# Kernel optimization log

Measured on AMD Instinct MI355X. Metric: run time of the kernel, lower is better.

Reference implementation:

```python
import jax, jax.numpy as jnp
import numpy as np

# ---- fixed configuration (see shape_source) ----
B, ND, NPR = 64, 32, 32          # batch, drug-subgraph nodes, protein-subgraph nodes
LD, LP = 100, 1000               # drug_MAX_LENGH, protein_MAX_LENGH
DIM, CONV = 64, 40               # char_dim, conv
DK, PK = (4, 6, 8), (4, 8, 12)   # drug_kernel, protein_kernel
VD, VP = 71, 26                  # SMILES / FASTA vocab sizes
ED, EP, EDP = 128, 128, 64       # DDI / PPI / DPI edges per subgraph
GNN_LAYERS = 2
SLOPE = 0.01                     # LeakyReLU default slope


def setup_inputs():
    key = jax.random.key(0)
    ks = iter(jax.random.split(key, 64))
    def nrm(shape, s=0.02):
        return jax.random.normal(next(ks), shape, jnp.float32) * s
    inp = {}
    inp['drug_tokens'] = jax.random.randint(next(ks), (B, LD), 0, VD, jnp.int32)
    inp['protein_tokens'] = jax.random.randint(next(ks), (B, LP), 0, VP, jnp.int32)
    inp['drug_node_tokens'] = jax.random.randint(next(ks), (B, ND, LD), 0, VD, jnp.int32)
    inp['protein_node_tokens'] = jax.random.randint(next(ks), (B, NPR, LP), 0, VP, jnp.int32)
    inp['ddi_edges'] = jax.random.randint(next(ks), (B, 2, ED), 0, ND, jnp.int32)
    inp['ppi_edges'] = jax.random.randint(next(ks), (B, 2, EP), 0, NPR, jnp.int32)
    inp['dpi_edges'] = jax.random.randint(next(ks), (B, 2, EDP), 0, min(ND, NPR), jnp.int32)
    # sequence embeddings (padding_idx=0 -> zero row)
    inp['drug_embed'] = nrm((VD, DIM)).at[0].set(0.)
    inp['protein_embed'] = nrm((VP, DIM)).at[0].set(0.)
    # drug CNN stack
    inp['dW1'], inp['db1'] = nrm((CONV, DIM, DK[0])), jnp.zeros((CONV,), jnp.float32)
    inp['dW2'], inp['db2'] = nrm((2*CONV, CONV, DK[1])), jnp.zeros((2*CONV,), jnp.float32)
    inp['dW3'], inp['db3'] = nrm((4*CONV, 2*CONV, DK[2])), jnp.zeros((4*CONV,), jnp.float32)
    # protein CNN stack
    inp['pW1'], inp['pb1'] = nrm((CONV, DIM, PK[0])), jnp.zeros((CONV,), jnp.float32)
    inp['pW2'], inp['pb2'] = nrm((2*CONV, CONV, PK[1])), jnp.zeros((2*CONV,), jnp.float32)
    inp['pW3'], inp['pb3'] = nrm((4*CONV, 2*CONV, PK[2])), jnp.zeros((4*CONV,), jnp.float32)
    # graph node-feature embedding tables (creat_drug_node / creat_protein_node)
    inp['drug_node_table'] = nrm((VD, LD)).at[0].set(0.)
    inp['protein_node_table'] = nrm((VP, LP)).at[0].set(0.)
    # SAGEConv params: Wl (neighbor path, has bias), Wr (root path, no bias)
    inp['ddi_Wl'], inp['ddi_bl'], inp['ddi_Wr'] = nrm((LD, LD)), jnp.zeros((LD,), jnp.float32), nrm((LD, LD))
    inp['ppi_Wl'], inp['ppi_bl'], inp['ppi_Wr'] = nrm((LP, LP)), jnp.zeros((LP,), jnp.float32), nrm((LP, LP))
    inp['dpi_Wl'], inp['dpi_bl'], inp['dpi_Wr'] = nrm((LP, LD)), jnp.zeros((LP,), jnp.float32), nrm((LP, LP))
    inp['pdi_Wl'], inp['pdi_bl'], inp['pdi_Wr'] = nrm((LD, LP)), jnp.zeros((LD,), jnp.float32), nrm((LD, LD))
    # fusion MLP
    inp['fc1_W'], inp['fc1_b'] = nrm((1024, 1420)), jnp.zeros((1024,), jnp.float32)
    inp['fc2_W'], inp['fc2_b'] = nrm((1024, 1024)), jnp.zeros((1024,), jnp.float32)
    inp['fc3_W'], inp['fc3_b'] = nrm((512, 1024)), jnp.zeros((512,), jnp.float32)
    inp['out_W'], inp['out_b'] = nrm((2, 512)), jnp.zeros((2,), jnp.float32)
    return inp


def _conv_relu(x, w, b):
    # x: [B, Cin, L], w: [Cout, Cin, K] -> valid Conv1d + ReLU
    y = jax.lax.conv_general_dilated(x, w, (1,), 'VALID',
                                     dimension_numbers=('NCH', 'OIH', 'NCH'))
    return jax.nn.relu(y + b[None, :, None])


def _node_feat(tokens, table, vocab):
    # mean over sequence of embedded tokens == (token-count histogram / L) @ table
    counts = jax.nn.one_hot(tokens, vocab, dtype=table.dtype).sum(axis=2)  # [B, N, V]
    return jnp.einsum('bnv,vd->bnd', counts, table) / tokens.shape[-1]


def _sage(xs, xd, edges, Wl, bl, Wr):
    # PyG SAGEConv, aggr='mean': lin_l(mean_j x_src[j]) + lin_r(x_dst)
    src, dst = edges[0], edges[1]
    n = xd.shape[0]
    s = jax.ops.segment_sum(xs[src], dst, num_segments=n)
    c = jax.ops.segment_sum(jnp.ones((src.shape[0],), xs.dtype), dst, num_segments=n)
    agg = s / jnp.maximum(c, 1.0)[:, None]
    return agg @ Wl.T + bl + xd @ Wr.T


def _forward(drug_tokens, protein_tokens, drug_node_tokens, protein_node_tokens,
             ddi_edges, ppi_edges, dpi_edges,
             drug_embed, protein_embed,
             dW1, db1, dW2, db2, dW3, db3,
             pW1, pb1, pW2, pb2, pW3, pb3,
             drug_node_table, protein_node_table,
             ddi_Wl, ddi_bl, ddi_Wr, ppi_Wl, ppi_bl, ppi_Wr,
             dpi_Wl, dpi_bl, dpi_Wr, pdi_Wl, pdi_bl, pdi_Wr,
             fc1_W, fc1_b, fc2_W, fc2_b, fc3_W, fc3_b, out_W, out_b):
    # --- CNN branches (maxpool kernel spans whole remaining length == global max) ---
    x = drug_embed[drug_tokens].transpose(0, 2, 1)            # [B, DIM, LD]
    for w, b in ((dW1, db1), (dW2, db2), (dW3, db3)):
        x = _conv_relu(x, w, b)
    drug_feat = x.max(axis=2)                                 # [B, 4*CONV]
    y = protein_embed[protein_tokens].transpose(0, 2, 1)      # [B, DIM, LP]
    for w, b in ((pW1, pb1), (pW2, pb2), (pW3, pb3)):
        y = _conv_relu(y, w, b)
    prot_feat = y.max(axis=2)                                 # [B, 4*CONV]
    # --- graph node features: mean over sequence of node-token embeddings ---
    dx = _node_feat(drug_node_tokens, drug_node_table, VD)    # [B, ND, LD]
    px = _node_feat(protein_node_tokens, protein_node_table, VP)  # [B, NPR, LP]
    # --- hetero SAGE message passing, aggr='mean' across relations ---
    def _hetero(dxi, pxi, ddi, ppi, dpi):
        pdi = dpi[::-1]
        d = 0.5 * (_sage(dxi, dxi, ddi, ddi_Wl, ddi_bl, ddi_Wr)
                   + _sage(pxi, dxi, pdi, pdi_Wl, pdi_bl, pdi_Wr))
        p = 0.5 * (_sage(pxi, pxi, ppi, ppi_Wl, ppi_bl, ppi_Wr)
                   + _sage(dxi, pxi, dpi, dpi_Wl, dpi_bl, dpi_Wr))
        return d, p
    hetero_b = jax.vmap(_hetero)
    for _ in range(GNN_LAYERS):
        dx, px = hetero_b(dx, px, ddi_edges, ppi_edges, dpi_edges)
    # node 0 of each subgraph is the query drug / protein
    graph_feat = jnp.concatenate([dx[:, 0], px[:, 0]], axis=-1)   # [B, LD+LP]
    # --- fusion MLP (dropout = identity at eval) ---
    pair = jnp.concatenate([drug_feat, prot_feat, graph_feat], axis=-1)  # [B, 1420]
    h = jax.nn.leaky_relu(pair @ fc1_W.T + fc1_b, SLOPE)
    h = jax.nn.leaky_relu(h @ fc2_W.T + fc2_b, SLOPE)
    h = jax.nn.leaky_relu(h @ fc3_W.T + fc3_b, SLOPE)
    return h @ out_W.T + out_b                                 # [B, 2]


def reference(drug_tokens, protein_tokens, drug_node_tokens, protein_node_tokens,
              ddi_edges, ppi_edges, dpi_edges,
              drug_embed, protein_embed,
              dW1, db1, dW2, db2, dW3, db3,
              pW1, pb1, pW2, pb2, pW3, pb3,
              drug_node_table, protein_node_table,
              ddi_Wl, ddi_bl, ddi_Wr, ppi_Wl, ppi_bl, ppi_Wr,
              dpi_Wl, dpi_bl, dpi_Wr, pdi_Wl, pdi_bl, pdi_Wr,
              fc1_W, fc1_b, fc2_W, fc2_b, fc3_W, fc3_b, out_W, out_b):
    return _forward(drug_tokens, protein_tokens, drug_node_tokens, protein_node_tokens,
                    ddi_edges, ppi_edges, dpi_edges,
                    drug_embed, protein_embed,
                    dW1, db1, dW2, db2, dW3, db3,
                    pW1, pb1, pW2, pb2, pW3, pb3,
                    drug_node_table, protein_node_table,
                    ddi_Wl, ddi_bl, ddi_Wr, ppi_Wl, ppi_bl, ppi_Wr,
                    dpi_Wl, dpi_bl, dpi_Wr, pdi_Wl, pdi_bl, pdi_Wr,
                    fc1_W, fc1_b, fc2_W, fc2_b, fc3_W, fc3_b, out_W, out_b)
```

## Files before the change

### kernel.cpp

```cpp
#include <hip/hip_runtime.h>
#include <hip/hip_bf16.h>


typedef __attribute__((ext_vector_type(8))) short short8;
typedef __attribute__((ext_vector_type(4))) float f32x4;
union FragU { uint32_t u[4]; uint4 q; short8 s; };

static __device__ inline unsigned short f2bf(float v) {
    __hip_bfloat16 h = __float2bfloat16(v);
    return *(unsigned short*)&h;
}

static constexpr size_t O_PAIR = 0;
static constexpr size_t O_CF1  = 363520;
static constexpr size_t O_CF2  = 625664;
static constexpr size_t O_CF3  = 887808;
static constexpr size_t O_BD   = 1018880;
static constexpr size_t O_BP   = 1019392;
static constexpr size_t O_WDS  = 1023488;
static constexpr size_t O_WPS  = 1342976;
static constexpr size_t O_WTP1 = 5864960;
static constexpr size_t O_WTP2 = 5930496;
static constexpr size_t O_WTP3 = 6012416;
static constexpr size_t O_WTD1 = 6503936;
static constexpr size_t O_WTD2 = 6569472;
static constexpr size_t O_WTD3 = 6651392;
static constexpr size_t AR     = 6897152;
static constexpr size_t A_AD  = AR + 0;
static constexpr size_t A_AP  = AR + 479232;
static constexpr size_t A_A2D = AR + 1327104;
static constexpr size_t A_A2P = AR + 1486848;
static constexpr size_t A_UD  = AR + 1769472;
static constexpr size_t A_UP  = AR + 1855488;
static constexpr size_t A_RHO = AR + 2641920;
static constexpr size_t A_Y2P = AR + 0;
static constexpr size_t A_Y1P = AR + 10158080;
static constexpr size_t A_Y1D = AR + 15278080;
static constexpr size_t A_Y2D = AR + 15810560;
static constexpr size_t NEED_BYTES = AR + 16793600;

__global__ void zero32_k(uint32_t* __restrict__ p, int n) {
    int i = blockIdx.x * 256 + threadIdx.x;
    if (i < n) p[i] = 0u;
}

static constexpr long Q0 = 100;
static constexpr long Q1 = Q0 + 1000;
static constexpr long Q2 = Q1 + 14336;
static constexpr long Q3 = Q2 + 14336;
static constexpr long Q4 = Q3 + 131072;
static constexpr long Q5 = Q4 + 1048576;
static constexpr long Q6 = Q5 + 1048576;
static constexpr long Q7 = Q6 + 163840;
static constexpr long Q8 = Q7 + 32768;
static constexpr long Q9 = Q8 + 40960;
static constexpr long Q10 = Q9 + 245760;
static constexpr long Q11 = Q10 + 32768;
static constexpr long Q12 = Q11 + 40960;
static constexpr long Q13 = Q12 + 122880;
static constexpr long Q14 = Q13 + 70400;
static constexpr long Q15 = Q14 + 20480;
static constexpr long Q16 = Q15 + 163840;
// ... 43 lines not shown
    if (idx < Q8)  { wtconv_block(WtP1, pW1, 40, 64, 4, 8, idx - Q7); return; }
    if (idx < Q9)  { wtconv_block(WtP2, pW2, 80, 40, 8, 8, idx - Q8); return; }
    if (idx < Q10) { wtconv_block(WtP3, pW3, 160, 80, 12, 16, idx - Q9); return; }
    if (idx < Q11) { wtconv_block(WtD1, dW1, 40, 64, 4, 8, idx - Q10); return; }
    if (idx < Q12) { wtconv_block(WtD2, dW2, 80, 40, 6, 8, idx - Q11); return; }
    if (idx < Q13) { wtconv_block(WtD3, dW3, 160, 80, 8, 8, idx - Q12); return; }
    if (idx < Q14) {
        long l = idx - Q13;
        int b = (int)(l / 1100), j = (int)(l % 1100);
        if (j < 100) pair[(size_t)b * 1420 + 320 + j] = 0.5f * (ddi_bl[j] + pdi_bl[j]);
        else { int j2 = j - 100; pair[(size_t)b * 1420 + 420 + j2] = 0.5f * (ppi_bl[j2] + dpi_bl[j2]); }
        return;
    }
    if (idx < Q15) {
        long l = idx - Q14;
        int b = (int)(l / 320), j = (int)(l % 320);
        pair[(size_t)b * 1420 + j] = 0.f;
        return;
    }
    if (idx < Q16) { cfz[idx - Q15] = 0.f; return; }
    if (idx < Q17) { gnnz[idx - Q16] = 0u; return; }
}

__global__ __launch_bounds__(256) void gnn_front_k(const int* __restrict__ ddi,
                                                   const int* __restrict__ ppi,
                                                   const int* __restrict__ dpi,
                                                   const int* __restrict__ dtoks,
                                                   const int* __restrict__ ptoks,
                                                   const float* __restrict__ dtable,
                                                   const float* __restrict__ ptable,
                                                   float* __restrict__ RHO,
                                                   unsigned short* __restrict__ Ad,
                                                   unsigned short* __restrict__ Ap) {
    const int role = blockIdx.x, b = blockIdx.y, tid = threadIdx.x;
    __shared__ float M[4][32][32];
    __shared__ int cnt4[4][32];
    __shared__ float inv4[4][32];
    __shared__ float W7[7][32];
    __shared__ int cnt[32][72];
    __shared__ float WC[7][72];
    for (int i = tid; i < 4 * 32 * 32; i += 256) ((float*)M)[i] = 0.f;
    if (tid < 128) ((int*)cnt4)[tid] = 0;
    __syncthreads();
    const int* ed = ddi + (size_t)b * 256;
    const int* ep = ppi + (size_t)b * 256;
    const int* ex = dpi + (size_t)b * 128;
    if (tid < 128) {
        atomicAdd(&cnt4[0][ed[128 + tid]], 1);
        atomicAdd(&cnt4[1][ep[128 + tid]], 1);
    } else if (tid < 192) {
        int e = tid - 128;
        atomicAdd(&cnt4[2][ex[e]], 1);
        atomicAdd(&cnt4[3][ex[64 + e]], 1);
    }
    __syncthreads();
    if (tid < 128) {
        int which = tid >> 5, j = tid & 31;
        inv4[which][j] = 1.f / (float)max(cnt4[which][j], 1);
    }
    __syncthreads();
    if (tid < 128) {
        int s = ed[tid], d = ed[128 + tid];
        atomicAdd(&M[0][d][s], inv4[0][d]);
        int s2 = ep[tid], d2 = ep[128 + tid];
        atomicAdd(&M[1][d2][s2], inv4[1][d2]);
    } else if (tid < 192) {
        int e = tid - 128;
        int dr = ex[e], pr = ex[64 + e];
        atomicAdd(&M[2][dr][pr], inv4[2][dr]);
        atomicAdd(&M[3][pr][dr], inv4[3][pr]);
    }
    __syncthreads();
    if (tid < 32) {
        int j = tid;
        if (role == 0) {
            float r1 = 0.f, r4 = 0.f, r5 = 0.f, r7 = 0.f;
            for (int k = 0; k < 32; ++k) {
                r1 += M[0][0][k] * M[0][k][j];
                r4 += M[2][0][k] * M[3][k][j];
                r5 += M[1][0][k] * M[3][k][j];
                r7 += M[3][0][k] * M[0][k][j];
            }
            W7[0][j] = r1; W7[1][j] = M[0][0][j]; W7[2][j] = (j == 0) ? 1.f : 0.f;
            W7[3][j] = r4; W7[4][j] = r5; W7[5][j] = M[3][0][j]; W7[6][j] = r7;
        } else {
            float s1 = 0.f, s3 = 0.f, s4 = 0.f, s7 = 0.f;
            for (int k = 0; k < 32; ++k) {
                s1 += M[0][0][k] * M[2][k][j];
                s3 += M[2][0][k] * M[1][k][j];
                s4 += M[1][0][k] * M[1][k][j];
                s7 += M[3][0][k] * M[2][k][j];
            }
            W7[0][j] = s1; W7[1][j] = M[2][0][j]; W7[2][j] = s3;
            W7[3][j] = s4; W7[4][j] = M[1][0][j];
            W7[5][j] = (j == 0) ? 1.f : 0.f; W7[6][j] = s7;
        }
    }
    if (role == 0 && tid == 0) {
        float a = 0.f, bq = 0.f, cq = 0.f, dq = 0.f;
        for (int k = 0; k < 32; ++k) {
            a += M[0][0][k]; bq += M[2][0][k]; cq += M[1][0][k]; dq += M[3][0][k];
        }
        RHO[b * 4 + 0] = a; RHO[b * 4 + 1] = bq; RHO[b * 4 + 2] = cq; RHO[b * 4 + 3] = dq;
    }
    const int V = role ? 26 : 71;
    const int L = role ? 1000 : 100;
    for (int i = tid; i < 32 * 72; i += 256) ((int*)cnt)[i] = 0;
    __syncthreads();
    const int* tk = (role ? ptoks : dtoks) + (size_t)b * 32 * L;
    for (int i = tid; i < 32 * L; i += 256) atomicAdd(&cnt[i / L][tk[i]], 1);
    __syncthreads();
    float invL = 1.f / (float)L;
    for (int o = tid; o < 7 * V; o += 256) {
        int i = o / V, v = o % V;
        float a = 0.f;
        for (int k = 0; k < 32; ++k) a += W7[i][k] * (float)cnt[k][v];
        WC[i][v] = a * invL;
    }
    __syncthreads();
    size_t g0d = (size_t)b * 1248, g1d_ = (size_t)(64 + b) * 1248, g2d = (size_t)(128 + b) * 1248;
    size_t g0p = (size_t)b * 2208, g1p = (size_t)(64 + b) * 2208, g2p = (size_t)(128 + b) * 2208;
    if (role == 0) {
        int d = tid;
        if (d >= 100) return;
        float acc[7] = {};
        for (int v = 0; v < 71; ++v) {
            float tv = dtable[(size_t)v * 100 + d];
            #pragma unroll
            for (int i = 0; i < 7; ++i) acc[i] += WC[i][v] * tv;
        }
        unsigned short h;
        h = f2bf(acc[0]); Ad[g0d + d] = h;
        h = f2bf(acc[1]); Ad[g0d + 112 + d] = h; Ad[g1d_ + d] = h;
        h = f2bf(acc[2]); Ad[g1d_ + 112 + d] = h;
        h = f2bf(acc[3]); Ap[g0p + 2048 + d] = h;
        h = f2bf(acc[4]); Ap[g1p + 2048 + d] = h;
        h = f2bf(acc[5]); Ap[g2p + 2048 + d] = h; Ad[g2d + 112 + d] = h;
        h = f2bf(acc[6]); Ad[g2d + d] = h;
    } else {
        for (int d = tid; d < 1000; d += 256) {
            float acc[7] = {};
            for (int v = 0; v < 26; ++v) {
                float tv = ptable[(size_t)v * 1000 + d];
                #pragma unroll
                for (int i = 0; i < 7; ++i) acc[i] += WC[i][v] * tv;
            }
            unsigned short h;
            h = f2bf(acc[0]); Ad[g0d + 224 + d] = h;
            h = f2bf(acc[1]); Ad[g1d_ + 224 + d] = h; Ap[g0p + 1024 + d] = h;
            h = f2bf(acc[2]); Ap[g0p + d] = h;
            h = f2bf(acc[3]); Ap[g1p + d] = h;
            h = f2bf(acc[4]); Ap[g1p + 1024 + d] = h; Ap[g2p + d] = h;
            h = f2bf(acc[5]); Ap[g2p + 1024 + d] = h;
            h = f2bf(acc[6]); Ad[g2d + 224 + d] = h;
        }
    }
}

__device__ __forceinline__ void sk_body(const unsigned short* __restrict__ A, int lda,
                                        const unsigned short* __restrict__ Bm, int ldb,
                                        int K, int KS, float scale,
                                        float* __restrict__ out,
                                        int rs, int coloff, int Nw,
                                        int bx, int by, int gz) {
    const int tid = threadIdx.x;
    const int lane = tid & 63, w = tid >> 6, c = lane & 15, q = lane >> 4;
    const int n = bx * 64 + w * 16 + c;
    const unsigned short* Ab = A + (size_t)gz * 64 * lda;
// ... 3 lines not shown
    f32x4 acc[4];
    #pragma unroll
    for (int i = 0; i < 4; ++i) acc[i] = (f32x4){0.f, 0.f, 0.f, 0.f};
    for (int k = k0; k < k1; k += 32) {
        FragU bf;
        bf.q = *(const uint4*)&Bm[(size_t)n * ldb + k + q * 8];
        #pragma unroll
        for (int i = 0; i < 4; ++i) {
            FragU af;
            af.q = *(const uint4*)&Ab[(size_t)(i * 16 + c) * lda + k + q * 8];
            acc[i] = __builtin_amdgcn_mfma_f32_16x16x32_bf16(af.s, bf.s, acc[i], 0, 0, 0);
        }
    }
    if (n >= Nw) return;
    #pragma unroll
    for (int i = 0; i < 4; ++i)
        #pragma unroll
        for (int r = 0; r < 4; ++r) {
            int m = gz * 64 + i * 16 + q * 4 + r;
            atomicAdd(&out[(size_t)m * rs + coloff + n], scale * acc[i][r]);
        }
}

__global__ __launch_bounds__(256) void sk_stage1(const unsigned short* __restrict__ Ad,
                                                 const unsigned short* __restrict__ WdS,
                                                 float* __restrict__ Ud,
                                                 const unsigned short* __restrict__ Ap,
                                                 const unsigned short* __restrict__ WpS,
                                                 float* __restrict__ Up) {
    int z = blockIdx.z;
    if (z < 3) {
        sk_body(Ap, 2208, WpS, 2208, 2208, 8, 0.5f, Up, 1024, 0, 1000,
                blockIdx.x, blockIdx.y, z);
    } else {
        if (blockIdx.x >= 2) return;
        sk_body(Ad, 1248, WdS, 1248, 1248, 8, 0.5f, Ud, 112, 0, 100,
                blockIdx.x, blockIdx.y, z - 3);
    }
}

__global__ __launch_bounds__(256) void sk_stage2(const unsigned short* __restrict__ A2d,
                                                 const unsigned short* __restrict__ WdS,
                                                 const unsigned short* __restrict__ A2p,
                                                 const unsigned short* __restrict__ WpS,
                                                 float* __restrict__ pair) {
    int z = blockIdx.z;
    if (z == 0) {
        sk_body(A2p, 2208, WpS, 2208, 2208, 8, 0.5f, pair, 1420, 420, 1000,
                blockIdx.x, blockIdx.y, 0);
    } else {
        if (blockIdx.x >= 2) return;
        sk_body(A2d, 1248, WdS, 1248, 1248, 8, 0.5f, pair, 1420, 320, 100,
                blockIdx.x, blockIdx.y, 0);
    }
}

__global__ void ep_k(const float* __restrict__ Ud, const float* __restrict__ Up,
                     const float* __restrict__ RHO,
                     const float* __restrict__ bd, const float* __restrict__ bp,
                     unsigned short* __restrict__ A2d, unsigned short* __restrict__ A2p) {
    int idx = blockIdx.x * 256 + threadIdx.x;
    if (idx < 192 * 112) {
        int m = idx / 112, n = idx % 112;
        if (n >= 100) return;
        int g = m >> 6, b = m & 63;
        float rho = (g == 0) ? RHO[b * 4 + 0] : (g == 1) ? 1.f : RHO[b * 4 + 3];
        unsigned short h = f2bf(Ud[idx] + rho * bd[n]);
        if (g == 0) A2d[(size_t)b * 1248 + n] = h;
        else if (g == 1) A2d[(size_t)b * 1248 + 112 + n] = h;
        else A2p[(size_t)b * 2208 + 2048 + n] = h;
    } else {
        int l = idx - 192 * 112;
        if (l >= 192 * 1024) return;
        int m = l / 1024, n = l % 1024;
        if (n >= 1000) return;
        int g = m >> 6, b = m & 63;
        float rho = (g == 0) ? RHO[b * 4 + 1] : (g == 1) ? RHO[b * 4 + 2] : 1.f;
        unsigned short h = f2bf(Up[l] + rho * bp[n]);
        if (g == 0) A2d[(size_t)b * 1248 + 224 + n] = h;
        else if (g == 1) A2p[(size_t)b * 2208 + n] = h;
        else A2p[(size_t)b * 2208 + 1024 + n] = h;
    }
}

template <int KP>
__device__ __forceinline__ void conv_body(const unsigned short* __restrict__ xin,
                                          int Ci, int Lp,
                                          const unsigned short* __restrict__ Wt, int KK,
                                          int nchunk,
                                          const float* __restrict__ bias, int Co,
                                          unsigned short* __restrict__ yout,
                                          int Lout, int LoutPad,
                                          float* __restrict__ pool, int pool_coloff,
                                          int b, int co0, int t0,
                                          unsigned short* As, unsigned short* xraw) {
    constexpr int CIPC = 64 / KP;
    constexpr int LG = (KP == 8) ? 3 : 4;
    const int tid = threadIdx.x;
    const int lane = tid & 63, w = tid >> 6, c = lane & 15, q = lane >> 4;
    f32x4 acc[4][4];
    #pragma unroll
    for (int i = 0; i < 4; ++i)
        #pragma unroll
        for (int j = 0; j < 4; ++j) acc[i][j] = (f32x4){0.f, 0.f, 0.f, 0.f};
    const int row8 = tid >> 3, col8 = (tid & 7) * 8;
    for (int ch = 0; ch < nchunk; ++ch) {
        const int kkbase = ch * 64, ci0 = ch * CIPC;
        #pragma unroll
        for (int p = 0; p < 2; ++p) {
            int row = row8 + p * 32;
            *(uint4*)&As[row * 72 + col8] =
                *(const uint4*)&Wt[(size_t)(co0 + row) * KK + kkbase + col8];
        }
        for (int gi = tid; gi < CIPC * 34; gi += 256) {
            int ci = gi / 34, g8 = (gi % 34) * 8, gt = t0 + g8;
            const unsigned short* src = xin + ((size_t)b * Ci + ci0 + ci) * Lp + gt;
// ... 18 lines not shown
            const int k0 = koff & (KP - 1);
            const uint32_t* xr = (const uint32_t*)xraw + cioff * 136;
            #pragma unroll
            for (int j = 0; j < 4; ++j) {
                int tt = w * 64 + j * 16 + c;
                int eoff = tt + k0;
                int d0 = eoff >> 1;
                unsigned sh = (unsigned)(eoff & 1) * 16u;
                uint32_t u0 = xr[d0], u1 = xr[d0 + 1], u2 = xr[d0 + 2],
                         u3 = xr[d0 + 3], u4 = xr[d0 + 4];
                FragU bf;
                bf.u[0] = __builtin_amdgcn_alignbit(u1, u0, sh);
                bf.u[1] = __builtin_amdgcn_alignbit(u2, u1, sh);
                bf.u[2] = __builtin_amdgcn_alignbit(u3, u2, sh);
                bf.u[3] = __builtin_amdgcn_alignbit(u4, u3, sh);
                #pragma unroll
                for (int i = 0; i < 4; ++i)
                    acc[i][j] = __builtin_amdgcn_mfma_f32_16x16x32_bf16(af[i].s, bf.s,
                                                                        acc[i][j], 0, 0, 0);
            }
        }
        __syncthreads();
    }
    if (pool) {
        #pragma unroll
        for (int i = 0; i < 4; ++i) {
            #pragma unroll
            for (int r = 0; r < 4; ++r) {
                int co = co0 + i * 16 + q * 4 + r;
                float bv = (co < Co) ? bias[co] : 0.f;
                float v = 0.f;
                #pragma unroll
                for (int j = 0; j < 4; ++j) {
                    int t = t0 + w * 64 + j * 16 + c;
                    if (t < Lout) v = fmaxf(v, fmaxf(acc[i][j][r] + bv, 0.f));
                }
                v = fmaxf(v, __shfl_xor(v, 1));
                v = fmaxf(v, __shfl_xor(v, 2));
                v = fmaxf(v, __shfl_xor(v, 4));
                v = fmaxf(v, __shfl_xor(v, 8));
                if (c == 0 && co < Co)
                    atomicMax((int*)&pool[(size_t)b * 1420 + pool_coloff + co],
                              __float_as_int(v));
            }
        }
    } else {
        #pragma unroll
        for (int i = 0; i < 4; ++i) {
            #pragma unroll
            for (int r = 0; r < 4; ++r) {
                int co = co0 + i * 16 + q * 4 + r;
                if (co >= Co) continue;
                float bv = bias[co];
                #pragma unroll
                for (int j = 0; j < 4; ++j) {
                    int t = t0 + w * 64 + j * 16 + c;
                    if (t < Lout) {
                        yout[((size_t)b * Co + co) * LoutPad + t] =
                            f2bf(fmaxf(acc[i][j][r] + bv, 0.f));
                    } else if (t < LoutPad) {
                        yout[((size_t)b * Co + co) * LoutPad + t] = 0;
                    }
                }
            }
        }
// ... 70 lines not shown
        __syncthreads();
    }
    #pragma unroll
    for (int i = 0; i < 4; ++i) {
        #pragma unroll
        for (int r = 0; r < 4; ++r) {
            int co = co0 + i * 16 + q * 4 + r;
            if (co >= Co) continue;
            float bv = bias[co];
            #pragma unroll
            for (int j = 0; j < 4; ++j) {
                int t = t0 + w * 64 + j * 16 + c;
                if (t < Lout) {
                    yout[((size_t)b * Co + co) * LoutPad + t] =
                        f2bf(fmaxf(acc[i][j][r] + bv, 0.f));
                } else if (t < LoutPad) {
                    yout[((size_t)b * Co + co) * LoutPad + t] = 0;
                }
            }
        }
    }
}

__global__ __launch_bounds__(256) void conv1_dual(
    const int* __restrict__ ptoks, const float* __restrict__ ptable,
    const unsigned short* __restrict__ WtP1, const float* __restrict__ pb1,
    unsigned short* __restrict__ y1p,
    const int* __restrict__ dtoks, const float* __restrict__ dtable,
    const unsigned short* __restrict__ WtD1, const float* __restrict__ db1,
    unsigned short* __restrict__ y1d) {
    __shared__ __align__(16) unsigned short As[64 * 72];
    __shared__ __align__(16) unsigned short xraw[8 * 272];
    __shared__ unsigned short tabT[64 * 72];
    __shared__ int tok_s[272];
    int z = blockIdx.z;
    if (z < 64) {
        conv1e_body(ptoks, ptable, 26, 1000, WtP1, 512, pb1, 40, y1p, 997, 1000,
                    z, 0, blockIdx.x * 256, As, xraw, tabT, tok_s);
    } else {
        if (blockIdx.x > 0) return;
        conv1e_body(dtoks, dtable, 71, 100, WtD1, 512, db1, 40, y1d, 97, 104,
                    z - 64, 0, 0, As, xraw, tabT, tok_s);
    }
}

__global__ __launch_bounds__(256) void conv2_dual(
    const unsigned short* __restrict__ y1p, const unsigned short* __restrict__ WtP2,
    const float* __restrict__ pb2, unsigned short* __restrict__ y2p,
    const unsigned short* __restrict__ y1d, const unsigned short* __restrict__ WtD2,
    const float* __restrict__ db2, unsigned short* __restrict__ y2d) {
    __shared__ __align__(16) unsigned short As[64 * 72];
    __shared__ __align__(16) unsigned short xraw[8 * 272];
    int z = blockIdx.z;
    if (z < 64) {
        conv_body<8>(y1p, 40, 1000, WtP2, 320, 5, pb2, 80, y2p, 990, 992,
                     nullptr, 0, z, blockIdx.y * 64, blockIdx.x * 256, As, xraw);
    } else {
        if (blockIdx.x > 0) return;
        conv_body<8>(y1d, 40, 104, WtD2, 320, 5, db2, 80, y2d, 92, 96,
                     nullptr, 0, z - 64, blockIdx.y * 64, 0, As, xraw);
    }
}

__global__ __launch_bounds__(256) void conv3_dual(
    const unsigned short* __restrict__ y2p, const unsigned short* __restrict__ WtP3,
    const float* __restrict__ pb3, float* __restrict__ pair,
    const unsigned short* __restrict__ y2d, const unsigned short* __restrict__ WtD3,
    const float* __restrict__ db3) {
    __shared__ __align__(16) unsigned short As[64 * 72];
    __shared__ __align__(16) unsigned short xraw[8 * 272];
    int z = blockIdx.z;
    if (z < 64) {
        conv_body<16>(y2p, 80, 992, WtP3, 1280, 20, pb3, 160, nullptr, 979, 0,
                      pair, 160, z, blockIdx.y * 64, blockIdx.x * 256, As, xraw);
    } else {
        if (blockIdx.x > 0) return;
        conv_body<8>(y2d, 80, 96, WtD3, 640, 10, db3, 160, nullptr, 85, 0,
                     pair, 0, z - 64, blockIdx.y * 64, 0, As, xraw);
    }
}

__global__ __launch_bounds__(256) void gemm_nt(const float* __restrict__ A, int lda,
                                               const float* __restrict__ Aep_b,
                                               const float* __restrict__ Bm,
                                               float* __restrict__ Cout,
                                               int M, int N, int K, int KC) {
    const int m0 = blockIdx.x * 64, n0 = blockIdx.y * 64, s = blockIdx.z;
    const int tid = threadIdx.x, ty = tid >> 4, tx = tid & 15;
    __shared__ __align__(16) float As[16][68];
    __shared__ __align__(16) float Bs[16][68];
    float acc[4][4] = {};
    const int kbeg = s * KC, kend = min(K, kbeg + KC);
    for (int k0 = kbeg; k0 < kend; k0 += 16) {
        int colk = k0 + tx;
        bool kok = colk < kend;
        #pragma unroll
        for (int qq = 0; qq < 4; ++qq) {
            int mi = ty + qq * 16;
            float va = 0.f;
            if (kok && (m0 + mi) < M) {
                va = A[(size_t)(m0 + mi) * lda + colk];
// ... 67 lines not shown
    const float* protein_embed   = (const float*)d_in[8];
    const float* dW1 = (const float*)d_in[9];  const float* db1 = (const float*)d_in[10];
    const float* dW2 = (const float*)d_in[11]; const float* db2 = (const float*)d_in[12];
    const float* dW3 = (const float*)d_in[13]; const float* db3 = (const float*)d_in[14];
    const float* pW1 = (const float*)d_in[15]; const float* pb1 = (const float*)d_in[16];
    const float* pW2 = (const float*)d_in[17]; const float* pb2 = (const float*)d_in[18];
    const float* pW3 = (const float*)d_in[19]; const float* pb3 = (const float*)d_in[20];
    const float* drug_node_table = (const float*)d_in[21];
    const float* prot_node_table = (const float*)d_in[22];
    const float* ddi_Wl = (const float*)d_in[23]; const float* ddi_bl = (const float*)d_in[24];
    const float* ddi_Wr = (const float*)d_in[25];
    const float* ppi_Wl = (const float*)d_in[26]; const float* ppi_bl = (const float*)d_in[27];
    const float* ppi_Wr = (const float*)d_in[28];
    const float* dpi_Wl = (const float*)d_in[29]; const float* dpi_bl = (const float*)d_in[30];
    const float* dpi_Wr = (const float*)d_in[31];
    const float* pdi_Wl = (const float*)d_in[32]; const float* pdi_bl = (const float*)d_in[33];
    const float* pdi_Wr = (const float*)d_in[34];
    const float* fc1_W = (const float*)d_in[35]; const float* fc1_b = (const float*)d_in[36];
    const float* fc2_W = (const float*)d_in[37]; const float* fc2_b = (const float*)d_in[38];
    const float* fc3_W = (const float*)d_in[39]; const float* fc3_b = (const float*)d_in[40];
    const float* out_W = (const float*)d_in[41]; const float* out_b = (const float*)d_in[42];

    float* outp = (float*)d_out;
    if (ws_size < NEED_BYTES) {
        zero32_k<<<g1d(out_size), 256, 0, stream>>>((uint32_t*)outp, out_size);
        return;
    }
    char* wsb = (char*)d_ws;
    float* pair = (float*)(wsb + O_PAIR);
    float* cf1 = (float*)(wsb + O_CF1); float* cf2 = (float*)(wsb + O_CF2);
    float* cf3 = (float*)(wsb + O_CF3);
    float* bd = (float*)(wsb + O_BD); float* bp = (float*)(wsb + O_BP);
    unsigned short* WdS  = (unsigned short*)(wsb + O_WDS);
    unsigned short* WpS  = (unsigned short*)(wsb + O_WPS);
    unsigned short* WtP1 = (unsigned short*)(wsb + O_WTP1);
    unsigned short* WtP2 = (unsigned short*)(wsb + O_WTP2);
    unsigned short* WtP3 = (unsigned short*)(wsb + O_WTP3);
    unsigned short* WtD1 = (unsigned short*)(wsb + O_WTD1);
    unsigned short* WtD2 = (unsigned short*)(wsb + O_WTD2);
    unsigned short* WtD3 = (unsigned short*)(wsb + O_WTD3);
    unsigned short* Ad  = (unsigned short*)(wsb + A_AD);
    unsigned short* Ap  = (unsigned short*)(wsb + A_AP);
    unsigned short* A2d = (unsigned short*)(wsb + A_A2D);
    unsigned short* A2p = (unsigned short*)(wsb + A_A2P);
    float* Ud  = (float*)(wsb + A_UD);
    float* Up  = (float*)(wsb + A_UP);
    float* RHO = (float*)(wsb + A_RHO);
    unsigned short* y2p = (unsigned short*)(wsb + A_Y2P);
    unsigned short* y1p = (unsigned short*)(wsb + A_Y1P);
    unsigned short* y1d = (unsigned short*)(wsb + A_Y1D);
    unsigned short* y2d = (unsigned short*)(wsb + A_Y2D);

    prep_k<<<g1d((int)Q17), 256, 0, stream>>>(bd, bp, WdS, WpS,
                                              WtP1, WtP2, WtP3, WtD1, WtD2, WtD3,
                                              pair, cf1, (uint32_t*)(wsb + A_AD),
                                              ddi_Wl, ddi_bl, ddi_Wr,
                                              ppi_Wl, ppi_bl, ppi_Wr,
                                              dpi_Wl, dpi_bl, dpi_Wr,
                                              pdi_Wl, pdi_bl, pdi_Wr,
                                              dW1, dW2, dW3, pW1, pW2, pW3);

    gnn_front_k<<<dim3(2, 64), 256, 0, stream>>>(ddi_edges, ppi_edges, dpi_edges,
                                                 drug_node_tokens, protein_node_toks,
                                                 drug_node_table, prot_node_table,
                                                 RHO, Ad, Ap);

    sk_stage1<<<dim3(16, 8, 6), 256, 0, stream>>>(Ad, WdS, Ud, Ap, WpS, Up);
    ep_k<<<g1d(192 * 112 + 192 * 1024), 256, 0, stream>>>(Ud, Up, RHO, bd, bp, A2d, A2p);
    sk_stage2<<<dim3(16, 8, 2), 256, 0, stream>>>(A2d, WdS, A2p, WpS, pair);

    conv1_dual<<<dim3(4, 1, 128), 256, 0, stream>>>(protein_tokens, protein_embed,
                                                    WtP1, pb1, y1p,
                                                    drug_tokens, drug_embed,
                                                    WtD1, db1, y1d);
    conv2_dual<<<dim3(4, 2, 128), 256, 0, stream>>>(y1p, WtP2, pb2, y2p,
                                                    y1d, WtD2, db2, y2d);
    conv3_dual<<<dim3(4, 3, 128), 256, 0, stream>>>(y2p, WtP3, pb3, pair,
                                                    y2d, WtD3, db3);

    gemm_nt<<<dim3(1, 16, 16), 256, 0, stream>>>(pair, 1420, nullptr, fc1_W, cf1,
                                                 64, 1024, 1420, kc_of(1420, 16));
    gemm_nt<<<dim3(1, 16, 16), 256, 0, stream>>>(cf1, 1024, fc1_b, fc2_W, cf2,
                                                 64, 1024, 1024, kc_of(1024, 16));
    gemm_nt<<<dim3(1, 8, 16), 256, 0, stream>>>(cf2, 1024, fc2_b, fc3_W, cf3,
                                                64, 512, 1024, kc_of(1024, 16));
    out_k<<<dim3(1), 128, 0, stream>>>(cf3, fc3_b, out_W, out_b, outp);
}
```

Measured before the change: 464.9 us.

## Co-schedule GNN branch stages with CNN conv stages in merged kernels

Merges the GNN front, first SK stage and epilogue kernels with the three CNN conv kernels into three combined launches whose blocks pick a role by block index. The two independent branches then share each launch, filling the GPU and cutting launch count. To make this possible the conv activations are moved to a separate workspace region so they do not overlap the GNN buffers. When the workspace is too small a fallback runs the two branches in sequence. The shared-memory pool is sized to the largest role, which may lower occupancy for the conv blocks.

```diff
diff --git a/kernel.cpp b/kernel.cpp
--- a/kernel.cpp
+++ b/kernel.cpp
@@ -33,11 +33,13 @@
 static constexpr size_t A_UD  = AR + 1769472;
 static constexpr size_t A_UP  = AR + 1855488;
 static constexpr size_t A_RHO = AR + 2641920;
-static constexpr size_t A_Y2P = AR + 0;
-static constexpr size_t A_Y1P = AR + 10158080;
-static constexpr size_t A_Y1D = AR + 15278080;
-static constexpr size_t A_Y2D = AR + 15810560;
-static constexpr size_t NEED_BYTES = AR + 16793600;
+static constexpr size_t GNN_END = AR + 2642944;
+static constexpr size_t SZ_Y2P = 10158080;
+static constexpr size_t SZ_Y1P = 5120000;
+static constexpr size_t SZ_Y1D = 532480;
+static constexpr size_t SZ_Y2D = 983040;
+static constexpr size_t NEED_FB   = AR + SZ_Y2P + SZ_Y1P + SZ_Y1D + SZ_Y2D;
+static constexpr size_t NEED_FULL = GNN_END + SZ_Y2P + SZ_Y1P + SZ_Y1D + SZ_Y2D;
 
 __global__ void zero32_k(uint32_t* __restrict__ p, int n) {
     int i = blockIdx.x * 256 + threadIdx.x;
@@ -127,53 +129,47 @@
     if (idx < Q17) { gnnz[idx - Q16] = 0u; return; }
 }
 
-__global__ __launch_bounds__(256) void gnn_front_k(const int* __restrict__ ddi,
-                                                   const int* __restrict__ ppi,
-                                                   const int* __restrict__ dpi,
-                                                   const int* __restrict__ dtoks,
-                                                   const int* __restrict__ ptoks,
-                                                   const float* __restrict__ dtable,
-                                                   const float* __restrict__ ptable,
-                                                   float* __restrict__ RHO,
-                                                   unsigned short* __restrict__ Ad,
-                                                   unsigned short* __restrict__ Ap) {
-    const int role = blockIdx.x, b = blockIdx.y, tid = threadIdx.x;
-    __shared__ float M[4][32][32];
-    __shared__ int cnt4[4][32];
-    __shared__ float inv4[4][32];
-    __shared__ float W7[7][32];
-    __shared__ int cnt[32][72];
-    __shared__ float WC[7][72];
-    for (int i = tid; i < 4 * 32 * 32; i += 256) ((float*)M)[i] = 0.f;
-    if (tid < 128) ((int*)cnt4)[tid] = 0;
+__device__ void gnn_front_body(const int* __restrict__ ddi, const int* __restrict__ ppi,
+                               const int* __restrict__ dpi,
+                               const int* __restrict__ dtoks, const int* __restrict__ ptoks,
+                               const float* __restrict__ dtable, const float* __restrict__ ptable,
+                               float* __restrict__ RHO,
+                               unsigned short* __restrict__ Ad, unsigned short* __restrict__ Ap,
+                               int role, int b, char* pool) {
+    const int tid = threadIdx.x;
+    float* M    = (float*)pool;
+    int*   cnt4 = (int*)(pool + 16384);
+    float* inv4 = (float*)(pool + 16896);
+    float* W7   = (float*)(pool + 17408);
+    int*   cnt  = (int*)(pool + 18304);
+    float* WC   = (float*)(pool + 27520);
+    for (int i = tid; i < 4 * 32 * 32; i += 256) M[i] = 0.f;
+    if (tid < 128) cnt4[tid] = 0;
     __syncthreads();
     const int* ed = ddi + (size_t)b * 256;
     const int* ep = ppi + (size_t)b * 256;
     const int* ex = dpi + (size_t)b * 128;
     if (tid < 128) {
-        atomicAdd(&cnt4[0][ed[128 + tid]], 1);
-        atomicAdd(&cnt4[1][ep[128 + tid]], 1);
+        atomicAdd(&cnt4[0 * 32 + ed[128 + tid]], 1);
+        atomicAdd(&cnt4[1 * 32 + ep[128 + tid]], 1);
     } else if (tid < 192) {
         int e = tid - 128;
-        atomicAdd(&cnt4[2][ex[e]], 1);
-        atomicAdd(&cnt4[3][ex[64 + e]], 1);
+        atomicAdd(&cnt4[2 * 32 + ex[e]], 1);
+        atomicAdd(&cnt4[3 * 32 + ex[64 + e]], 1);
     }
     __syncthreads();
-    if (tid < 128) {
-        int which = tid >> 5, j = tid & 31;
-        inv4[which][j] = 1.f / (float)max(cnt4[which][j], 1);
-    }
+    if (tid < 128) inv4[tid] = 1.f / (float)max(cnt4[tid], 1);
     __syncthreads();
     if (tid < 128) {
         int s = ed[tid], d = ed[128 + tid];
-        atomicAdd(&M[0][d][s], inv4[0][d]);
+        atomicAdd(&M[0 * 1024 + d * 32 + s], inv4[0 * 32 + d]);
         int s2 = ep[tid], d2 = ep[128 + tid];
-        atomicAdd(&M[1][d2][s2], inv4[1][d2]);
+        atomicAdd(&M[1 * 1024 + d2 * 32 + s2], inv4[1 * 32 + d2]);
     } else if (tid < 192) {
         int e = tid - 128;
         int dr = ex[e], pr = ex[64 + e];
-        atomicAdd(&M[2][dr][pr], inv4[2][dr]);
-        atomicAdd(&M[3][pr][dr], inv4[3][pr]);
+        atomicAdd(&M[2 * 1024 + dr * 32 + pr], inv4[2 * 32 + dr]);
+        atomicAdd(&M[3 * 1024 + pr * 32 + dr], inv4[3 * 32 + pr]);
     }
     __syncthreads();
     if (tid < 32) {
@@ -181,46 +177,50 @@
         if (role == 0) {
             float r1 = 0.f, r4 = 0.f, r5 = 0.f, r7 = 0.f;
             for (int k = 0; k < 32; ++k) {
-                r1 += M[0][0][k] * M[0][k][j];
-                r4 += M[2][0][k] * M[3][k][j];
-                r5 += M[1][0][k] * M[3][k][j];
-                r7 += M[3][0][k] * M[0][k][j];
-            }
-            W7[0][j] = r1; W7[1][j] = M[0][0][j]; W7[2][j] = (j == 0) ? 1.f : 0.f;
-            W7[3][j] = r4; W7[4][j] = r5; W7[5][j] = M[3][0][j]; W7[6][j] = r7;
+                r1 += M[0 * 1024 + 0 * 32 + k] * M[0 * 1024 + k * 32 + j];
+                r4 += M[2 * 1024 + 0 * 32 + k] * M[3 * 1024 + k * 32 + j];
+                r5 += M[1 * 1024 + 0 * 32 + k] * M[3 * 1024 + k * 32 + j];
+                r7 += M[3 * 1024 + 0 * 32 + k] * M[0 * 1024 + k * 32 + j];
+            }
+            W7[0 * 32 + j] = r1; W7[1 * 32 + j] = M[0 * 1024 + j];
+            W7[2 * 32 + j] = (j == 0) ? 1.f : 0.f;
+            W7[3 * 32 + j] = r4; W7[4 * 32 + j] = r5;
+            W7[5 * 32 + j] = M[3 * 1024 + j]; W7[6 * 32 + j] = r7;
         } else {
             float s1 = 0.f, s3 = 0.f, s4 = 0.f, s7 = 0.f;
             for (int k = 0; k < 32; ++k) {
-                s1 += M[0][0][k] * M[2][k][j];
-                s3 += M[2][0][k] * M[1][k][j];
-                s4 += M[1][0][k] * M[1][k][j];
-                s7 += M[3][0][k] * M[2][k][j];
-            }
-            W7[0][j] = s1; W7[1][j] = M[2][0][j]; W7[2][j] = s3;
-            W7[3][j] = s4; W7[4][j] = M[1][0][j];
-            W7[5][j] = (j == 0) ? 1.f : 0.f; W7[6][j] = s7;
+                s1 += M[0 * 1024 + 0 * 32 + k] * M[2 * 1024 + k * 32 + j];
+                s3 += M[2 * 1024 + 0 * 32 + k] * M[1 * 1024 + k * 32 + j];
+                s4 += M[1 * 1024 + 0 * 32 + k] * M[1 * 1024 + k * 32 + j];
+                s7 += M[3 * 1024 + 0 * 32 + k] * M[2 * 1024 + k * 32 + j];
+            }
+            W7[0 * 32 + j] = s1; W7[1 * 32 + j] = M[2 * 1024 + j];
+            W7[2 * 32 + j] = s3; W7[3 * 32 + j] = s4;
+            W7[4 * 32 + j] = M[1 * 1024 + j];
+            W7[5 * 32 + j] = (j == 0) ? 1.f : 0.f; W7[6 * 32 + j] = s7;
         }
     }
     if (role == 0 && tid == 0) {
         float a = 0.f, bq = 0.f, cq = 0.f, dq = 0.f;
         for (int k = 0; k < 32; ++k) {
-            a += M[0][0][k]; bq += M[2][0][k]; cq += M[1][0][k]; dq += M[3][0][k];
+            a += M[0 * 1024 + k]; bq += M[2 * 1024 + k];
+            cq += M[1 * 1024 + k]; dq += M[3 * 1024 + k];
         }
         RHO[b * 4 + 0] = a; RHO[b * 4 + 1] = bq; RHO[b * 4 + 2] = cq; RHO[b * 4 + 3] = dq;
     }
     const int V = role ? 26 : 71;
     const int L = role ? 1000 : 100;
-    for (int i = tid; i < 32 * 72; i += 256) ((int*)cnt)[i] = 0;
+    for (int i = tid; i < 32 * 72; i += 256) cnt[i] = 0;
     __syncthreads();
     const int* tk = (role ? ptoks : dtoks) + (size_t)b * 32 * L;
-    for (int i = tid; i < 32 * L; i += 256) atomicAdd(&cnt[i / L][tk[i]], 1);
+    for (int i = tid; i < 32 * L; i += 256) atomicAdd(&cnt[(i / L) * 72 + tk[i]], 1);
     __syncthreads();
     float invL = 1.f / (float)L;
     for (int o = tid; o < 7 * V; o += 256) {
         int i = o / V, v = o % V;
         float a = 0.f;
-        for (int k = 0; k < 32; ++k) a += W7[i][k] * (float)cnt[k][v];
-        WC[i][v] = a * invL;
+        for (int k = 0; k < 32; ++k) a += W7[i * 32 + k] * (float)cnt[k * 72 + v];
+        WC[i * 72 + v] = a * invL;
     }
     __syncthreads();
     size_t g0d = (size_t)b * 1248, g1d_ = (size_t)(64 + b) * 1248, g2d = (size_t)(128 + b) * 1248;
@@ -232,7 +232,7 @@
         for (int v = 0; v < 71; ++v) {
             float tv = dtable[(size_t)v * 100 + d];
             #pragma unroll
-            for (int i = 0; i < 7; ++i) acc[i] += WC[i][v] * tv;
+            for (int i = 0; i < 7; ++i) acc[i] += WC[i * 72 + v] * tv;
         }
         unsigned short h;
         h = f2bf(acc[0]); Ad[g0d + d] = h;
@@ -248,7 +248,7 @@
             for (int v = 0; v < 26; ++v) {
                 float tv = ptable[(size_t)v * 1000 + d];
                 #pragma unroll
-                for (int i = 0; i < 7; ++i) acc[i] += WC[i][v] * tv;
+                for (int i = 0; i < 7; ++i) acc[i] += WC[i * 72 + v] * tv;
             }
             unsigned short h;
             h = f2bf(acc[0]); Ad[g0d + 224 + d] = h;
@@ -298,44 +298,10 @@
         }
 }
 
-__global__ __launch_bounds__(256) void sk_stage1(const unsigned short* __restrict__ Ad,
-                                                 const unsigned short* __restrict__ WdS,
-                                                 float* __restrict__ Ud,
-                                                 const unsigned short* __restrict__ Ap,
-                                                 const unsigned short* __restrict__ WpS,
-                                                 float* __restrict__ Up) {
-    int z = blockIdx.z;
-    if (z < 3) {
-        sk_body(Ap, 2208, WpS, 2208, 2208, 8, 0.5f, Up, 1024, 0, 1000,
-                blockIdx.x, blockIdx.y, z);
-    } else {
-        if (blockIdx.x >= 2) return;
-        sk_body(Ad, 1248, WdS, 1248, 1248, 8, 0.5f, Ud, 112, 0, 100,
-                blockIdx.x, blockIdx.y, z - 3);
-    }
-}
-
-__global__ __launch_bounds__(256) void sk_stage2(const unsigned short* __restrict__ A2d,
-                                                 const unsigned short* __restrict__ WdS,
-                                                 const unsigned short* __restrict__ A2p,
-                                                 const unsigned short* __restrict__ WpS,
-                                                 float* __restrict__ pair) {
-    int z = blockIdx.z;
-    if (z == 0) {
-        sk_body(A2p, 2208, WpS, 2208, 2208, 8, 0.5f, pair, 1420, 420, 1000,
-                blockIdx.x, blockIdx.y, 0);
-    } else {
-        if (blockIdx.x >= 2) return;
-        sk_body(A2d, 1248, WdS, 1248, 1248, 8, 0.5f, pair, 1420, 320, 100,
-                blockIdx.x, blockIdx.y, 0);
-    }
-}
-
-__global__ void ep_k(const float* __restrict__ Ud, const float* __restrict__ Up,
-                     const float* __restrict__ RHO,
-                     const float* __restrict__ bd, const float* __restrict__ bp,
-                     unsigned short* __restrict__ A2d, unsigned short* __restrict__ A2p) {
-    int idx = blockIdx.x * 256 + threadIdx.x;
+__device__ void ep_item(int idx, const float* __restrict__ Ud, const float* __restrict__ Up,
+                        const float* __restrict__ RHO,
+                        const float* __restrict__ bd, const float* __restrict__ bp,
+                        unsigned short* __restrict__ A2d, unsigned short* __restrict__ A2p) {
     if (idx < 192 * 112) {
         int m = idx / 112, n = idx % 112;
         if (n >= 100) return;
@@ -367,7 +333,7 @@
                                           const float* __restrict__ bias, int Co,
                                           unsigned short* __restrict__ yout,
                                           int Lout, int LoutPad,
-                                          float* __restrict__ pool, int pool_coloff,
+                                          float* __restrict__ pool_out, int pool_coloff,
                                           int b, int co0, int t0,
                                           unsigned short* As, unsigned short* xraw) {
     constexpr int CIPC = 64 / KP;
@@ -432,7 +398,7 @@
         }
         __syncthreads();
     }
-    if (pool) {
+    if (pool_out) {
         #pragma unroll
         for (int i = 0; i < 4; ++i) {
             #pragma unroll
@@ -450,7 +416,7 @@
                 v = fmaxf(v, __shfl_xor(v, 4));
                 v = fmaxf(v, __shfl_xor(v, 8));
                 if (c == 0 && co < Co)
-                    atomicMax((int*)&pool[(size_t)b * 1420 + pool_coloff + co],
+                    atomicMax((int*)&pool_out[(size_t)b * 1420 + pool_coloff + co],
                               __float_as_int(v));
             }
         }
@@ -567,61 +533,108 @@
     }
 }
 
-__global__ __launch_bounds__(256) void conv1_dual(
-    const int* __restrict__ ptoks, const float* __restrict__ ptable,
-    const unsigned short* __restrict__ WtP1, const float* __restrict__ pb1,
-    unsigned short* __restrict__ y1p,
-    const int* __restrict__ dtoks, const float* __restrict__ dtable,
-    const unsigned short* __restrict__ WtD1, const float* __restrict__ db1,
-    unsigned short* __restrict__ y1d) {
-    __shared__ __align__(16) unsigned short As[64 * 72];
-    __shared__ __align__(16) unsigned short xraw[8 * 272];
-    __shared__ unsigned short tabT[64 * 72];
-    __shared__ int tok_s[272];
+__global__ __launch_bounds__(256) void m1_k(int nconv,
+    const int* ptoks, const float* ptable, const unsigned short* WtP1,
+    const float* pb1, unsigned short* y1p,
+    const int* dtoks, const float* dtable, const unsigned short* WtD1,
+    const float* db1, unsigned short* y1d,
+    const int* ddi, const int* ppi, const int* dpi,
+    const int* dntoks, const int* pntoks,
+    const float* dntable, const float* pntable,
+    float* RHO, unsigned short* Ad, unsigned short* Ap) {
+    __shared__ __align__(16) char pool[29568];
+    int id = blockIdx.x;
+    if (id < nconv) {
+        unsigned short* As = (unsigned short*)pool;
+        unsigned short* xraw = (unsigned short*)(pool + 9216);
+        unsigned short* tabT = (unsigned short*)(pool + 13568);
+        int* tok_s = (int*)(pool + 22784);
+        if (id < 256) {
+            conv1e_body(ptoks, ptable, 26, 1000, WtP1, 512, pb1, 40, y1p, 997, 1000,
+                        id >> 2, 0, (id & 3) * 256, As, xraw, tabT, tok_s);
+        } else {
+            conv1e_body(dtoks, dtable, 71, 100, WtD1, 512, db1, 40, y1d, 97, 104,
+                        id - 256, 0, 0, As, xraw, tabT, tok_s);
+        }
+    } else {
+        int t = id - nconv;
+        gnn_front_body(ddi, ppi, dpi, dntoks, pntoks, dntable, pntable,
+                       RHO, Ad, Ap, t >> 6, t & 63, pool);
+    }
+}
+
+__global__ __launch_bounds__(256) void m2_k(int nconv,
+    const unsigned short* y1p, const unsigned short* WtP2, const float* pb2,
+    unsigned short* y2p,
+    const unsigned short* y1d, const unsigned short* WtD2, const float* db2,
+    unsigned short* y2d,
+    const unsigned short* Ad, const unsigned short* WdS, float* Ud,
+    const unsigned short* Ap, const unsigned short* WpS, float* Up) {
+    __shared__ __align__(16) char pool[13568];
+    int id = blockIdx.x;
+    if (id < nconv) {
+        unsigned short* As = (unsigned short*)pool;
+        unsigned short* xraw = (unsigned short*)(pool + 9216);
+        if (id < 512) {
+            conv_body<8>(y1p, 40, 1000, WtP2, 320, 5, pb2, 80, y2p, 990, 992,
+                         nullptr, 0, id >> 3, ((id >> 2) & 1) * 64, (id & 3) * 256, As, xraw);
+        } else {
+            int t = id - 512;
+            conv_body<8>(y1d, 40, 104, WtD2, 320, 5, db2, 80, y2d, 92, 96,
+                         nullptr, 0, t >> 1, (t & 1) * 64, 0, As, xraw);
+        }
+    } else {
+        int t = id - nconv;
+        int bx = t & 15, by = (t >> 4) & 7, bz = t >> 7;
+        if (bz < 3) {
+            sk_body(Ap, 2208, WpS, 2208, 2208, 8, 0.5f, Up, 1024, 0, 1000, bx, by, bz);
+        } else {
+            if (bx >= 2) return;
+            sk_body(Ad, 1248, WdS, 1248, 1248, 8, 0.5f, Ud, 112, 0, 100, bx, by, bz - 3);
+        }
+    }
+}
+
+__global__ __launch_bounds__(256) void m3_k(int nconv,
+    const unsigned short* y2p, const unsigned short* WtP3, const float* pb3,
+    float* pair,
+    const unsigned short* y2d, const unsigned short* WtD3, const float* db3,
+    const float* Ud, const float* Up, const float* RHO,
+    const float* bd, const float* bp,
+    unsigned short* A2d, unsigned short* A2p) {
+    __shared__ __align__(16) char pool[13568];
+    int id = blockIdx.x;
+    if (id < nconv) {
+        unsigned short* As = (unsigned short*)pool;
+        unsigned short* xraw = (unsigned short*)(pool + 9216);
+        if (id < 768) {
+            int z = id / 12, r = id % 12;
+            conv_body<16>(y2p, 80, 992, WtP3, 1280, 20, pb3, 160, nullptr, 979, 0,
+                          pair, 160, z, (r >> 2) * 64, (r & 3) * 256, As, xraw);
+        } else {
+            int t = id - 768;
+            conv_body<8>(y2d, 80, 96, WtD3, 640, 10, db3, 160, nullptr, 85, 0,
+                         pair, 0, t / 3, (t % 3) * 64, 0, As, xraw);
+        }
+    } else {
+        int idx = (id - nconv) * 256 + threadIdx.x;
+        ep_item(idx, Ud, Up, RHO, bd, bp, A2d, A2p);
+    }
+}
+
+__global__ __launch_bounds__(256) void sk_stage2(const unsigned short* __restrict__ A2d,
+                                                 const unsigned short* __restrict__ WdS,
+                                                 const unsigned short* __restrict__ A2p,
+                                                 const unsigned short* __restrict__ WpS,
+                                                 float* __restrict__ pair) {
     int z = blockIdx.z;
-    if (z < 64) {
-        conv1e_body(ptoks, ptable, 26, 1000, WtP1, 512, pb1, 40, y1p, 997, 1000,
-                    z, 0, blockIdx.x * 256, As, xraw, tabT, tok_s);
+    if (z == 0) {
+        sk_body(A2p, 2208, WpS, 2208, 2208, 8, 0.5f, pair, 1420, 420, 1000,
+                blockIdx.x, blockIdx.y, 0);
     } else {
-        if (blockIdx.x > 0) return;
-        conv1e_body(dtoks, dtable, 71, 100, WtD1, 512, db1, 40, y1d, 97, 104,
-                    z - 64, 0, 0, As, xraw, tabT, tok_s);
-    }
-}
-
-__global__ __launch_bounds__(256) void conv2_dual(
-    const unsigned short* __restrict__ y1p, const unsigned short* __restrict__ WtP2,
-    const float* __restrict__ pb2, unsigned short* __restrict__ y2p,
-    const unsigned short* __restrict__ y1d, const unsigned short* __restrict__ WtD2,
-    const float* __restrict__ db2, unsigned short* __restrict__ y2d) {
-    __shared__ __align__(16) unsigned short As[64 * 72];
-    __shared__ __align__(16) unsigned short xraw[8 * 272];
-    int z = blockIdx.z;
-    if (z < 64) {
-        conv_body<8>(y1p, 40, 1000, WtP2, 320, 5, pb2, 80, y2p, 990, 992,
-                     nullptr, 0, z, blockIdx.y * 64, blockIdx.x * 256, As, xraw);
-    } else {
-        if (blockIdx.x > 0) return;
-        conv_body<8>(y1d, 40, 104, WtD2, 320, 5, db2, 80, y2d, 92, 96,
-                     nullptr, 0, z - 64, blockIdx.y * 64, 0, As, xraw);
-    }
-}
-
-__global__ __launch_bounds__(256) void conv3_dual(
-    const unsigned short* __restrict__ y2p, const unsigned short* __restrict__ WtP3,
-    const float* __restrict__ pb3, float* __restrict__ pair,
-    const unsigned short* __restrict__ y2d, const unsigned short* __restrict__ WtD3,
-    const float* __restrict__ db3) {
-    __shared__ __align__(16) unsigned short As[64 * 72];
-    __shared__ __align__(16) unsigned short xraw[8 * 272];
-    int z = blockIdx.z;
-    if (z < 64) {
-        conv_body<16>(y2p, 80, 992, WtP3, 1280, 20, pb3, 160, nullptr, 979, 0,
-                      pair, 160, z, blockIdx.y * 64, blockIdx.x * 256, As, xraw);
-    } else {
-        if (blockIdx.x > 0) return;
-        conv_body<8>(y2d, 80, 96, WtD3, 640, 10, db3, 160, nullptr, 85, 0,
-                     pair, 0, z - 64, blockIdx.y * 64, 0, As, xraw);
+        if (blockIdx.x >= 2) return;
+        sk_body(A2d, 1248, WdS, 1248, 1248, 8, 0.5f, pair, 1420, 320, 100,
+                blockIdx.x, blockIdx.y, 0);
     }
 }
 
@@ -735,10 +748,12 @@
     const float* out_W = (const float*)d_in[41]; const float* out_b = (const float*)d_in[42];
 
     float* outp = (float*)d_out;
-    if (ws_size < NEED_BYTES) {
+    if (ws_size < NEED_FB) {
         zero32_k<<<g1d(out_size), 256, 0, stream>>>((uint32_t*)outp, out_size);
         return;
     }
+    const bool full = (ws_size >= NEED_FULL);
+
     char* wsb = (char*)d_ws;
     float* pair = (float*)(wsb + O_PAIR);
     float* cf1 = (float*)(wsb + O_CF1); float* cf2 = (float*)(wsb + O_CF2);
@@ -759,10 +774,11 @@
     float* Ud  = (float*)(wsb + A_UD);
     float* Up  = (float*)(wsb + A_UP);
     float* RHO = (float*)(wsb + A_RHO);
-    unsigned short* y2p = (unsigned short*)(wsb + A_Y2P);
-    unsigned short* y1p = (unsigned short*)(wsb + A_Y1P);
-    unsigned short* y1d = (unsigned short*)(wsb + A_Y1D);
-    unsigned short* y2d = (unsigned short*)(wsb + A_Y2D);
+    size_t cbase = full ? GNN_END : AR;
+    unsigned short* y2p = (unsigned short*)(wsb + cbase);
+    unsigned short* y1p = (unsigned short*)(wsb + cbase + SZ_Y2P);
+    unsigned short* y1d = (unsigned short*)(wsb + cbase + SZ_Y2P + SZ_Y1P);
+    unsigned short* y2d = (unsigned short*)(wsb + cbase + SZ_Y2P + SZ_Y1P + SZ_Y1D);
 
     prep_k<<<g1d((int)Q17), 256, 0, stream>>>(bd, bp, WdS, WpS,
                                               WtP1, WtP2, WtP3, WtD1, WtD2, WtD3,
@@ -773,23 +789,44 @@
                                               pdi_Wl, pdi_bl, pdi_Wr,
                                               dW1, dW2, dW3, pW1, pW2, pW3);
 
-    gnn_front_k<<<dim3(2, 64), 256, 0, stream>>>(ddi_edges, ppi_edges, dpi_edges,
-                                                 drug_node_tokens, protein_node_toks,
-                                                 drug_node_table, prot_node_table,
-                                                 RHO, Ad, Ap);
-
-    sk_stage1<<<dim3(16, 8, 6), 256, 0, stream>>>(Ad, WdS, Ud, Ap, WpS, Up);
-    ep_k<<<g1d(192 * 112 + 192 * 1024), 256, 0, stream>>>(Ud, Up, RHO, bd, bp, A2d, A2p);
-    sk_stage2<<<dim3(16, 8, 2), 256, 0, stream>>>(A2d, WdS, A2p, WpS, pair);
-
-    conv1_dual<<<dim3(4, 1, 128), 256, 0, stream>>>(protein_tokens, protein_embed,
-                                                    WtP1, pb1, y1p,
-                                                    drug_tokens, drug_embed,
-                                                    WtD1, db1, y1d);
-    conv2_dual<<<dim3(4, 2, 128), 256, 0, stream>>>(y1p, WtP2, pb2, y2p,
-                                                    y1d, WtD2, db2, y2d);
-    conv3_dual<<<dim3(4, 3, 128), 256, 0, stream>>>(y2p, WtP3, pb3, pair,
-                                                    y2d, WtD3, db3);
+    if (full) {
+        m1_k<<<dim3(320 + 128), 256, 0, stream>>>(320,
+            protein_tokens, protein_embed, WtP1, pb1, y1p,
+            drug_tokens, drug_embed, WtD1, db1, y1d,
+            ddi_edges, ppi_edges, dpi_edges, drug_node_tokens, protein_node_toks,
+            drug_node_table, prot_node_table, RHO, Ad, Ap);
+        m2_k<<<dim3(640 + 768), 256, 0, stream>>>(640,
+            y1p, WtP2, pb2, y2p, y1d, WtD2, db2, y2d,
+            Ad, WdS, Ud, Ap, WpS, Up);
+        m3_k<<<dim3(960 + 852), 256, 0, stream>>>(960,
+            y2p, WtP3, pb3, pair, y2d, WtD3, db3,
+            Ud, Up, RHO, bd, bp, A2d, A2p);
+        sk_stage2<<<dim3(16, 8, 2), 256, 0, stream>>>(A2d, WdS, A2p, WpS, pair);
+    } else {
+        m1_k<<<dim3(128), 256, 0, stream>>>(0,
+            protein_tokens, protein_embed, WtP1, pb1, y1p,
+            drug_tokens, drug_embed, WtD1, db1, y1d,
+            ddi_edges, ppi_edges, dpi_edges, drug_node_tokens, protein_node_toks,
+            drug_node_table, prot_node_table, RHO, Ad, Ap);
+        m2_k<<<dim3(768), 256, 0, stream>>>(0,
+            y1p, WtP2, pb2, y2p, y1d, WtD2, db2, y2d,
+            Ad, WdS, Ud, Ap, WpS, Up);
+        m3_k<<<dim3(852), 256, 0, stream>>>(0,
+            y2p, WtP3, pb3, pair, y2d, WtD3, db3,
+            Ud, Up, RHO, bd, bp, A2d, A2p);
+        sk_stage2<<<dim3(16, 8, 2), 256, 0, stream>>>(A2d, WdS, A2p, WpS, pair);
+        m1_k<<<dim3(320), 256, 0, stream>>>(320,
+            protein_tokens, protein_embed, WtP1, pb1, y1p,
+            drug_tokens, drug_embed, WtD1, db1, y1d,
+            ddi_edges, ppi_edges, dpi_edges, drug_node_tokens, protein_node_toks,
+            drug_node_table, prot_node_table, RHO, Ad, Ap);
+        m2_k<<<dim3(640), 256, 0, stream>>>(640,
+            y1p, WtP2, pb2, y2p, y1d, WtD2, db2, y2d,
+            Ad, WdS, Ud, Ap, WpS, Up);
+        m3_k<<<dim3(960), 256, 0, stream>>>(960,
+            y2p, WtP3, pb3, pair, y2d, WtD3, db3,
+            Ud, Up, RHO, bd, bp, A2d, A2p);
+    }
 
     gemm_nt<<<dim3(1, 16, 16), 256, 0, stream>>>(pair, 1420, nullptr, fc1_W, cf1,
                                                  64, 1024, 1420, kc_of(1420, 16));
```

After: 466.4 us. No clear change (+0.3%).
